# Optimization experiments

Measured on AMD Instinct MI355X. Metric: run time of the kernel, lower is better.

The kernel has to match this reference:

```python
import jax, jax.numpy as jnp
import numpy as np

N_NODES = 100000
N_EDGES = 1600000
D_IN = 128
D_OUT = 128
EPS = 1e-5


def setup_inputs() -> dict:
    key = jax.random.key(0)
    k1, k2, k3, k4, k5 = jax.random.split(key, 5)
    x = jax.random.normal(k1, (N_NODES, D_IN), dtype=jnp.float32)
    row = jax.random.randint(k2, (N_EDGES,), 0, N_NODES, dtype=jnp.int64)
    col = jax.random.randint(k3, (N_EDGES,), 0, N_NODES, dtype=jnp.int64)
    adj_vals = jax.random.uniform(k4, (N_EDGES,), dtype=jnp.float32)
    # Xavier-uniform init for weight, zeros for bias (as in the torch module)
    limit = float(np.sqrt(6.0 / (D_IN + D_OUT)))
    weight = jax.random.uniform(k5, (D_IN, D_OUT), minval=-limit, maxval=limit, dtype=jnp.float32)
    bias = jnp.zeros((D_OUT,), dtype=jnp.float32)
    return {"x": x, "row": row, "col": col, "adj_vals": adj_vals, "weight": weight, "bias": bias}


def reference(x, row, col, adj_vals, weight, bias):
    # degree = row-sum of sparse adj
    degree = jax.ops.segment_sum(adj_vals, row, num_segments=N_NODES)
    degree = jnp.where(degree == 0, EPS, degree)
    d_inv_sqrt = (degree + EPS) ** -0.5  # [N]
    # edge-wise symmetric normalization: D^-1/2 A D^-1/2
    edge_w = d_inv_sqrt[row] * adj_vals * d_inv_sqrt[col]  # [E]
    # SpMM: gather neighbor features, scale, scatter-add to destination rows
    msgs = edge_w[:, None] * x[col]  # [E, D_IN]
    agg = jax.ops.segment_sum(msgs, row, num_segments=N_NODES)  # [N, D_IN]
    return agg @ weight + bias
```

## Files before the change

kernel.cpp:

```cpp
#include <hip/hip_runtime.h>

#define NN 100000
#define NE 1600000
#define D  128
#define EPS 1e-5f

#define NBKT   782
#define NEB    391
#define EPB_H  4096
#define NSCAN  (NBKT*NEB)
#define GRID2  299
#define CAP    2560

#define OFF_HCNT 0x0000000ULL
#define OFF_PART 0x0140000ULL
#define OFF_DINV 0x0150000ULL
#define OFF_RBC  0x0200000ULL
#define OFF_GREC 0x0280000ULL
#define OFF_ECOL 0x0F00000ULL
#define OFF_YB   0x1700000ULL

typedef short short8 __attribute__((ext_vector_type(8)));
typedef float f32x4 __attribute__((ext_vector_type(4)));

static __device__ __forceinline__ unsigned f2bf(float f) {
    unsigned u = __float_as_uint(f);
    return (u + 0x7fffu + ((u >> 16) & 1u)) >> 16;
}

__global__ void k0h(const int* __restrict__ row, unsigned* __restrict__ hcnt) {
    __shared__ unsigned h[NBKT];
    int t = threadIdx.x, b = blockIdx.x;
    for (int i = t; i < NBKT; i += 256) h[i] = 0;
    __syncthreads();
    int ebeg = b * EPB_H;
    for (int i = t; i < EPB_H; i += 256) {
        int e = ebeg + i;
        if (e < NE) atomicAdd(&h[((unsigned)row[e]) >> 7], 1u);
    }
    __syncthreads();
    for (int i = t; i < NBKT; i += 256) hcnt[i * NEB + b] = h[i];
}

__global__ void k2a(const unsigned* __restrict__ hcnt, unsigned* __restrict__ part) {
    __shared__ unsigned s[256];
    int t = threadIdx.x;
    int gi = blockIdx.x * 1024 + t * 4;
    unsigned v = 0;
    #pragma unroll
    for (int j = 0; j < 4; ++j) if (gi + j < NSCAN) v += hcnt[gi + j];
    s[t] = v;
    __syncthreads();
    for (int d = 128; d > 0; d >>= 1) {
        if (t < d) s[t] += s[t + d];
        __syncthreads();
    }
    if (t == 0) part[blockIdx.x] = s[0];
}

__global__ void k2c(unsigned* __restrict__ hcnt, const unsigned* __restrict__ part) {
    __shared__ unsigned s[256];
    __shared__ unsigned bbase;
    int t = threadIdx.x, g = blockIdx.x;

    unsigned v = 0;
    for (int i = t; i < g; i += 256) v += part[i];
    s[t] = v;
    __syncthreads();
    for (int d = 128; d > 0; d >>= 1) {
        if (t < d) s[t] += s[t + d];
        __syncthreads();
    }
    if (t == 0) bbase = s[0];
    __syncthreads();
    unsigned base = bbase;
    __syncthreads();

    int gi = g * 1024 + t * 4;
    unsigned w[4], tot = 0;
    #pragma unroll
    for (int j = 0; j < 4; ++j) {
        w[j] = (gi + j < NSCAN) ? hcnt[gi + j] : 0;
        tot += w[j];
    }
    s[t] = tot;
    __syncthreads();
    for (int d = 1; d < 256; d <<= 1) {
        unsigned u = (t >= d) ? s[t - d] : 0;
        __syncthreads();
        s[t] += u;
        __syncthreads();
    }
    unsigned run = base + s[t] - tot;
    #pragma unroll
    for (int j = 0; j < 4; ++j) {
        if (gi + j < NSCAN) { hcnt[gi + j] = run; run += w[j]; }
    }
}

__launch_bounds__(256)
__global__ void k3(const int* __restrict__ row, const int* __restrict__ col,
                   const float* __restrict__ adj, const unsigned* __restrict__ hcnt,
                   unsigned long long* __restrict__ grec) {
    __shared__ unsigned cur[NBKT];
    int t = threadIdx.x, b = blockIdx.x;
    for (int i = t; i < NBKT; i += 256) cur[i] = hcnt[i * NEB + b];
    __syncthreads();
    int ebeg = b * EPB_H;
    for (int i = t; i < EPB_H; i += 256) {
        int e = ebeg + i;
        if (e >= NE) continue;
        unsigned r = (unsigned)row[e];
        unsigned aq = (unsigned)rintf(adj[e] * 32767.0f);
        unsigned lo = (unsigned)col[e] | (aq << 17);
        unsigned dst = atomicAdd(&cur[r >> 7], 1u);
        grec[dst] = (unsigned long long)lo | ((unsigned long long)(r & 127u) << 32);
    }
}

__launch_bounds__(256, 2)
__global__ void k1g(const float* __restrict__ x, const float* __restrict__ w,
                    const unsigned* __restrict__ hcnt,
                    const unsigned long long* __restrict__ grec,
                    float* __restrict__ dinv_g, unsigned* __restrict__ rbcnt_g,
                    unsigned* __restrict__ ecol_g, unsigned short* __restrict__ yb) {
    __shared__ unsigned short sx[128 * 128];
    __shared__ unsigned short sw[128 * 128];
    __shared__ unsigned sdeg[128], scnt[128], srb[128], scur[128];
    __shared__ float sdv[128];
    unsigned* secol = (unsigned*)sx;
    int tid = threadIdx.x;
    int b = blockIdx.x;
    int base = b * 128;

    if (tid < 128) { sdeg[tid] = 0; scnt[tid] = 0; }
    __syncthreads();
    unsigned beg = hcnt[b * NEB];
    unsigned end = (b == NBKT - 1) ? NE : hcnt[(b + 1) * NEB];
    unsigned n = end - beg;
    for (unsigned p = beg + tid; p < end; p += 256) {
        unsigned long long rec = grec[p];
        unsigned rid = (unsigned)(rec >> 32) & 127u;
        atomicAdd(&sdeg[rid], ((unsigned)rec >> 17) & 0x7FFFu);
        atomicAdd(&scnt[rid], 1u);
    }
    __syncthreads();

    if (tid < 128) {
        float d = (float)sdeg[tid] * (1.0f / 32767.0f);
        d = (d == 0.0f) ? EPS : d;
        float dv = rsqrtf(d + EPS);
        sdv[tid] = dv;
        int r = base + tid;
        if (r < NN) dinv_g[r] = dv;
        srb[tid] = scnt[tid];
    }
    __syncthreads();
    for (int dd = 1; dd < 128; dd <<= 1) {
        unsigned u = (tid >= dd && tid < 128) ? srb[tid - dd] : 0;
        __syncthreads();
        if (tid < 128) srb[tid] += u;
        __syncthreads();
    }
    if (tid < 128) {
        unsigned rb = srb[tid] - scnt[tid];
        srb[tid] = rb;
        scur[tid] = rb;
        rbcnt_g[b * 128 + tid] = (rb << 16) | scnt[tid];
    }
    __syncthreads();

    for (unsigned p = beg + tid; p < end; p += 256) {
        unsigned long long rec = grec[p];
        unsigned rank = atomicAdd(&scur[(unsigned)(rec >> 32) & 127u], 1u);
        if (rank < CAP) secol[rank] = (unsigned)rec;
    }
    __syncthreads();
    unsigned ns = min(n, (unsigned)CAP);
    for (unsigned i = tid; i < ns; i += 256) ecol_g[(size_t)b * CAP + i] = secol[i];
    __syncthreads();

    #pragma unroll
    for (int i = 0; i < 8; ++i) {
        int task = i * 256 + tid;
        int nn = task & 127, ko = task >> 7;
        const float* wp = w + (size_t)(ko * 8) * D + nn;
        uint4 pk;
        pk.x = f2bf(wp[0])     | (f2bf(wp[D])     << 16);
        pk.y = f2bf(wp[2 * D]) | (f2bf(wp[3 * D]) << 16);
        pk.z = f2bf(wp[4 * D]) | (f2bf(wp[5 * D]) << 16);
        pk.w = f2bf(wp[6 * D]) | (f2bf(wp[7 * D]) << 16);
        int idx = (nn * 128 + ko * 8) ^ ((nn & 7) << 3);
        *(uint4*)(&sw[idx]) = pk;
    }
    #pragma unroll
    for (int i = 0; i < 8; ++i) {
        int task = i * 256 + tid;
        int ko = task & 15, r = task >> 4;
        int gr = base + r;
        float4 f0 = make_float4(0.f, 0.f, 0.f, 0.f), f1 = f0;
        if (gr < NN) {
            const float* xp = x + (size_t)gr * D + ko * 8;
            f0 = *(const float4*)xp;
            f1 = *(const float4*)(xp + 4);
        }
        uint4 pk;
        pk.x = f2bf(f0.x) | (f2bf(f0.y) << 16);
        pk.y = f2bf(f0.z) | (f2bf(f0.w) << 16);
        pk.z = f2bf(f1.x) | (f2bf(f1.y) << 16);
        pk.w = f2bf(f1.z) | (f2bf(f1.w) << 16);
        int idx = (r * 128 + ko * 8) ^ ((r & 7) << 3);
        *(uint4*)(&sx[idx]) = pk;
    }
    __syncthreads();

    int wv = tid >> 6, l = tid & 63;
    int lr = l & 15, g = l >> 4;

    f32x4 acc[2][8];
    #pragma unroll
    for (int ti = 0; ti < 2; ++ti)
        #pragma unroll
        for (int tj = 0; tj < 8; ++tj)
            acc[ti][tj] = (f32x4){0.f, 0.f, 0.f, 0.f};

    #pragma unroll
    for (int kc = 0; kc < 4; ++kc) {
        int kb = kc * 32 + g * 8;
        short8 a[2], bb[8];
        #pragma unroll
        for (int ti = 0; ti < 2; ++ti) {
            int r0 = wv * 32 + ti * 16 + lr;
            a[ti] = *(const short8*)(&sx[(r0 * 128 + kb) ^ ((r0 & 7) << 3)]);
        }
        #pragma unroll
        for (int tj = 0; tj < 8; ++tj) {
            int n0 = tj * 16 + lr;
            bb[tj] = *(const short8*)(&sw[(n0 * 128 + kb) ^ ((n0 & 7) << 3)]);
        }
        #pragma unroll
        for (int ti = 0; ti < 2; ++ti)
            #pragma unroll
            for (int tj = 0; tj < 8; ++tj)
                acc[ti][tj] = __builtin_amdgcn_mfma_f32_16x16x32_bf16(
                    a[ti], bb[tj], acc[ti][tj], 0, 0, 0);
    }

    #pragma unroll
    for (int ti = 0; ti < 2; ++ti) {
        #pragma unroll
        for (int reg = 0; reg < 4; ++reg) {
            int lrow = wv * 32 + ti * 16 + g * 4 + reg;
            int gr = base + lrow;
            if (gr < NN) {
                float dv = sdv[lrow];
                #pragma unroll
                for (int tj = 0; tj < 8; ++tj)
                    yb[(size_t)gr * D + tj * 16 + lr] =
                        (unsigned short)f2bf(acc[ti][tj][reg] * dv);
            }
        }
    }
}

__launch_bounds__(512, 4)
__global__ void k4b(const unsigned* __restrict__ rbcnt_g, const unsigned* __restrict__ ecol_g,
                    const float* __restrict__ dinv, const unsigned short* __restrict__ yb,
                    const float* __restrict__ bias, float* __restrict__ out) {
    __shared__ unsigned ecol[CAP + 16];
    __shared__ unsigned rb_l[128], cnt_l[128];
    __shared__ unsigned nsh;
    int t = threadIdx.x, bid = blockIdx.x;
    int xcd = bid & 7;
    int ch  = xcd >> 2;
    int q   = (bid >> 3) * 4 + (xcd & 3);
    if (q >= NBKT) return;
    int cb = ch * 64;

    if (t < 128) {
        unsigned v = rbcnt_g[q * 128 + t];
        rb_l[t] = v >> 16;
        cnt_l[t] = v & 0xFFFFu;
        if (t == 127) nsh = min((v >> 16) + (v & 0xFFFFu), (unsigned)CAP);
    }
    __syncthreads();
    unsigned n = nsh;
    const unsigned* eg = ecol_g + (size_t)q * CAP;
    for (unsigned i = t; i < n; i += 512) ecol[i] = eg[i];
    __syncthreads();

    int grp = t >> 4, lq = t & 15;
    for (int k = 0; k < 4; ++k) {
        int rowlo = grp * 4 + k;
        int r = q * 128 + rowlo;
        if (r >= NN) continue;
        unsigned jb = rb_l[rowlo];
        unsigned jend = min(jb + cnt_l[rowlo], (unsigned)CAP);

        float a0 = 0.f, a1 = 0.f, a2 = 0.f, a3 = 0.f;

        for (unsigned j = jb; j < jend; j += 16) {
            unsigned ee[16];
            uint2 yq[16];
            float wv[16];
            int cm[16];
            #pragma unroll
            for (int u = 0; u < 16; ++u) ee[u] = ecol[j + u];
            #pragma unroll
            for (int u = 0; u < 16; ++u) cm[u] = min((int)(ee[u] & 0x1FFFFu), NN - 1);
            #pragma unroll
            for (int u = 0; u < 16; ++u)
                yq[u] = *(const uint2*)(yb + (size_t)cm[u] * D + cb + lq * 4);
            #pragma unroll
            for (int u = 0; u < 16; ++u)
                wv[u] = (j + u < jend) ? (float)(ee[u] >> 17) : 0.f;
            #pragma unroll
            for (int u = 0; u < 16; ++u) {
                a0 += wv[u] * __uint_as_float(yq[u].x << 16);
                a1 += wv[u] * __uint_as_float(yq[u].x & 0xffff0000u);
                a2 += wv[u] * __uint_as_float(yq[u].y << 16);
                a3 += wv[u] * __uint_as_float(yq[u].y & 0xffff0000u);
            }
        }

        float scale = dinv[r] * (1.0f / 32767.0f);
        float4 bb = ((const float4*)(bias + cb))[lq];
        float4 rr = make_float4(a0 * scale + bb.x, a1 * scale + bb.y,
                                a2 * scale + bb.z, a3 * scale + bb.w);
        ((float4*)(out + (size_t)r * D + cb))[lq] = rr;
    }
}

extern "C" void kernel_launch(void* const* d_in, const int* in_sizes, int n_in,
                              void* d_out, int out_size, void* d_ws, size_t ws_size,
                              hipStream_t stream) {
    const float* x    = (const float*)d_in[0];
    const int*   row  = (const int*)d_in[1];
    const int*   col  = (const int*)d_in[2];
    const float* adj  = (const float*)d_in[3];
    const float* wgt  = (const float*)d_in[4];
    const float* bias = (const float*)d_in[5];
    float* out = (float*)d_out;
    char*  ws  = (char*)d_ws;

    unsigned* hcnt  = (unsigned*)(ws + OFF_HCNT);
    unsigned* part  = (unsigned*)(ws + OFF_PART);
    float*    dinv  = (float*)(ws + OFF_DINV);
    unsigned* rbcnt = (unsigned*)(ws + OFF_RBC);
    unsigned long long* grec = (unsigned long long*)(ws + OFF_GREC);
    unsigned* ecolg = (unsigned*)(ws + OFF_ECOL);
    unsigned short* yb = (unsigned short*)(ws + OFF_YB);

    k0h<<<NEB, 256, 0, stream>>>(row, hcnt);
    k2a<<<GRID2, 256, 0, stream>>>(hcnt, part);
    k2c<<<GRID2, 256, 0, stream>>>(hcnt, part);
    k3 <<<NEB, 256, 0, stream>>>(row, col, adj, hcnt, grec);
    k1g<<<NBKT, 256, 0, stream>>>(x, wgt, hcnt, grec, dinv, rbcnt, ecolg, yb);
    k4b<<<1568, 512, 0, stream>>>(rbcnt, ecolg, dinv, yb, bias, out);
}
```

Measured before the change: 137.9 us.

## Slice transformed features into 16-column planes so each XCD gathers one slice

The transformed-feature buffer is now stored as eight planes of 16 bf16 columns each, not row-major with 128 columns. Each gather block handles one bucket and one slice, mapped by block index mod 8, so each XCD's L2 holds only a 3.2MB slice of the feature table. Each row is now handled by 4 threads with 8-edge unrolling instead of 16 threads over 4 rows. The trade-off is 8x more blocks, each reloading the bucket's edge list into shared memory, and each gather fetches only 32B per row.

```diff
diff --git a/kernel.cpp b/kernel.cpp
--- a/kernel.cpp
+++ b/kernel.cpp
@@ -11,6 +11,7 @@
 #define NSCAN  (NBKT*NEB)
 #define GRID2  299
 #define CAP    2560
+#define SLW    16
 
 #define OFF_HCNT 0x0000000ULL
 #define OFF_PART 0x0140000ULL
@@ -256,7 +257,7 @@
                 float dv = sdv[lrow];
                 #pragma unroll
                 for (int tj = 0; tj < 8; ++tj)
-                    yb[(size_t)gr * D + tj * 16 + lr] =
+                    yb[(size_t)tj * (NN * SLW) + (size_t)gr * SLW + lr] =
                         (unsigned short)f2bf(acc[ti][tj][reg] * dv);
             }
         }
@@ -265,17 +266,15 @@
 
 __launch_bounds__(512, 4)
 __global__ void k4b(const unsigned* __restrict__ rbcnt_g, const unsigned* __restrict__ ecol_g,
-                    const float* __restrict__ dinv, const unsigned short* __restrict__ yb,
+                    const float* __restrict__ dinv, const unsigned short* __restrict__ ybs,
                     const float* __restrict__ bias, float* __restrict__ out) {
-    __shared__ unsigned ecol[CAP + 16];
+    __shared__ unsigned ecol[CAP + 8];
     __shared__ unsigned rb_l[128], cnt_l[128];
     __shared__ unsigned nsh;
     int t = threadIdx.x, bid = blockIdx.x;
-    int xcd = bid & 7;
-    int ch  = xcd >> 2;
-    int q   = (bid >> 3) * 4 + (xcd & 3);
-    if (q >= NBKT) return;
-    int cb = ch * 64;
+    int s = bid & 7;
+    int q = bid >> 3;
+    const unsigned short* ys = ybs + (size_t)s * (NN * SLW);
 
     if (t < 128) {
         unsigned v = rbcnt_g[q * 128 + t];
@@ -289,46 +288,43 @@
     for (unsigned i = t; i < n; i += 512) ecol[i] = eg[i];
     __syncthreads();
 
-    int grp = t >> 4, lq = t & 15;
-    for (int k = 0; k < 4; ++k) {
-        int rowlo = grp * 4 + k;
-        int r = q * 128 + rowlo;
-        if (r >= NN) continue;
-        unsigned jb = rb_l[rowlo];
-        unsigned jend = min(jb + cnt_l[rowlo], (unsigned)CAP);
-
-        float a0 = 0.f, a1 = 0.f, a2 = 0.f, a3 = 0.f;
-
-        for (unsigned j = jb; j < jend; j += 16) {
-            unsigned ee[16];
-            uint2 yq[16];
-            float wv[16];
-            int cm[16];
-            #pragma unroll
-            for (int u = 0; u < 16; ++u) ee[u] = ecol[j + u];
-            #pragma unroll
-            for (int u = 0; u < 16; ++u) cm[u] = min((int)(ee[u] & 0x1FFFFu), NN - 1);
-            #pragma unroll
-            for (int u = 0; u < 16; ++u)
-                yq[u] = *(const uint2*)(yb + (size_t)cm[u] * D + cb + lq * 4);
-            #pragma unroll
-            for (int u = 0; u < 16; ++u)
-                wv[u] = (j + u < jend) ? (float)(ee[u] >> 17) : 0.f;
-            #pragma unroll
-            for (int u = 0; u < 16; ++u) {
-                a0 += wv[u] * __uint_as_float(yq[u].x << 16);
-                a1 += wv[u] * __uint_as_float(yq[u].x & 0xffff0000u);
-                a2 += wv[u] * __uint_as_float(yq[u].y << 16);
-                a3 += wv[u] * __uint_as_float(yq[u].y & 0xffff0000u);
-            }
-        }
-
-        float scale = dinv[r] * (1.0f / 32767.0f);
-        float4 bb = ((const float4*)(bias + cb))[lq];
-        float4 rr = make_float4(a0 * scale + bb.x, a1 * scale + bb.y,
-                                a2 * scale + bb.z, a3 * scale + bb.w);
-        ((float4*)(out + (size_t)r * D + cb))[lq] = rr;
-    }
+    int grp = t >> 2, lq = t & 3;
+    int r = q * 128 + grp;
+    if (r >= NN) return;
+    unsigned jb = rb_l[grp];
+    unsigned jend = min(jb + cnt_l[grp], (unsigned)CAP);
+
+    float a0 = 0.f, a1 = 0.f, a2 = 0.f, a3 = 0.f;
+
+    for (unsigned j = jb; j < jend; j += 8) {
+        unsigned ee[8];
+        uint2 yq[8];
+        float wv[8];
+        int cm[8];
+        #pragma unroll
+        for (int u = 0; u < 8; ++u) ee[u] = ecol[j + u];
+        #pragma unroll
+        for (int u = 0; u < 8; ++u) cm[u] = min((int)(ee[u] & 0x1FFFFu), NN - 1);
+        #pragma unroll
+        for (int u = 0; u < 8; ++u)
+            yq[u] = *(const uint2*)(ys + (size_t)cm[u] * SLW + lq * 4);
+        #pragma unroll
+        for (int u = 0; u < 8; ++u)
+            wv[u] = (j + u < jend) ? (float)(ee[u] >> 17) : 0.f;
+        #pragma unroll
+        for (int u = 0; u < 8; ++u) {
+            a0 += wv[u] * __uint_as_float(yq[u].x << 16);
+            a1 += wv[u] * __uint_as_float(yq[u].x & 0xffff0000u);
+            a2 += wv[u] * __uint_as_float(yq[u].y << 16);
+            a3 += wv[u] * __uint_as_float(yq[u].y & 0xffff0000u);
+        }
+    }
+
+    float scale = dinv[r] * (1.0f / 32767.0f);
+    float4 bb = *(const float4*)(bias + s * SLW + lq * 4);
+    float4 rr = make_float4(a0 * scale + bb.x, a1 * scale + bb.y,
+                            a2 * scale + bb.z, a3 * scale + bb.w);
+    *(float4*)(out + (size_t)r * D + s * SLW + lq * 4) = rr;
 }
 
 extern "C" void kernel_launch(void* const* d_in, const int* in_sizes, int n_in,
@@ -356,5 +352,5 @@
     k2c<<<GRID2, 256, 0, stream>>>(hcnt, part);
     k3 <<<NEB, 256, 0, stream>>>(row, col, adj, hcnt, grec);
     k1g<<<NBKT, 256, 0, stream>>>(x, wgt, hcnt, grec, dinv, rbcnt, ecolg, yb);
-    k4b<<<1568, 512, 0, stream>>>(rbcnt, ecolg, dinv, yb, bias, out);
-}
+    k4b<<<NBKT * 8, 512, 0, stream>>>(rbcnt, ecolg, dinv, yb, bias, out);
+}
```

Result: slower. 150.0 us (+8.7%).
